# Kernel optimization log

Measured on AMD Instinct MI355X. Metric: run time of the kernel, lower is better.

## Reference

```python
import jax, jax.numpy as jnp
import numpy as np

B, D, NINC = 2097152, 16, 1000


def _make_map(key):
    # Build a valid adaptive map: per-dim monotone grid on [0,1] with NINC increments.
    w = jax.random.uniform(key, (D, NINC), dtype=jnp.float32) + 0.1  # positive widths
    inc = w / jnp.sum(w, axis=1, keepdims=True)                      # rows sum to 1
    grid = jnp.concatenate([jnp.zeros((D, 1), jnp.float32), jnp.cumsum(inc, axis=1)], axis=1)
    inc = grid[:, 1:] - grid[:, :-1]  # exact consistency: inc[d,i] = grid[d,i+1]-grid[d,i]
    return grid, inc


def setup_inputs() -> dict:
    key = jax.random.key(0)
    k1, k2 = jax.random.split(key)
    y = jax.random.uniform(k1, (B, D), dtype=jnp.float32)
    grid, inc = _make_map(k2)
    return {"y": y, "grid": grid, "inc": inc, "ninc": NINC}


def reference(y, grid, inc, ninc):
    # y: [B, D] in [0,1); grid: [D, ninc+1]; inc: [D, ninc]
    y_ninc = y * ninc                      # [B, D]
    iy = jnp.floor(y_ninc).astype(jnp.int32)
    dy_ninc = y_ninc - iy                  # fractional part within bin
    mask = iy < ninc                       # in-range bins (iy == ninc only when y == 1.0)
    iy_c = jnp.clip(iy, 0, ninc - 1)       # safe gather index
    d_idx = jnp.arange(y.shape[1])[None, :]  # [1, D]
    g = grid[d_idx, iy_c]                  # [B, D] left knot
    ig = inc[d_idx, iy_c]                  # [B, D] bin width
    # piecewise-linear affine map, predicated instead of boolean-mask scatter
    x = jnp.where(mask, g + ig * dy_ninc, grid[:, ninc][None, :])
    fac = jnp.where(mask, ig, inc[:, ninc - 1][None, :]) * ninc
    jac = jnp.prod(fac, axis=1)            # [B]
    return x, jac
```

## Files before the change

kernel.cpp:

```cpp
#include <hip/hip_runtime.h>


#define DIMS 16
#define NINC 1000
#define GROW (NINC + 1)
#define GTOT (DIMS * GROW)
#define BLOCK 1024
#define ROWS_PER_BLOCK 4096
#define NBLOCKS 512

__global__ __launch_bounds__(BLOCK, 8) void vegas_map_kernel(
    const float* __restrict__ y,
    const float* __restrict__ grid,
    float* __restrict__ x_out,
    float* __restrict__ jac_out,
    int B)
{
    __shared__ float sgrid[GTOT];

    {
        const float4* g4 = reinterpret_cast<const float4*>(grid);
        float4* s4 = reinterpret_cast<float4*>(sgrid);
        #pragma unroll
        for (int i = threadIdx.x; i < GTOT / 4; i += BLOCK)
            s4[i] = g4[i];
    }
    __syncthreads();

    const int base = blockIdx.x * ROWS_PER_BLOCK;

    #pragma unroll
    for (int it = 0; it < ROWS_PER_BLOCK / BLOCK; ++it) {
        const int b = base + it * BLOCK + threadIdx.x;
        if (b >= B) break;

        const float4* y4 = reinterpret_cast<const float4*>(y + (size_t)b * DIMS);
        float xs[DIMS];
        float jac = 1.0f;

        #pragma unroll
        for (int q = 0; q < 4; ++q) {
            float4 yv = y4[q];
            float ys[4] = {yv.x, yv.y, yv.z, yv.w};
            #pragma unroll
            for (int j = 0; j < 4; ++j) {
                const int d = q * 4 + j;
                float yn = ys[j] * (float)NINC;
                float fi = floorf(yn);
                int   iy = (int)fi;
                float dy = yn - (float)iy;
                int   iyc = iy < 0 ? 0 : (iy > NINC - 1 ? NINC - 1 : iy);
                const int sb = d * GROW + iyc;

                float xv, fac;
                if (iy < NINC) {
                    float g0 = sgrid[sb];
                    float g1 = sgrid[sb + 1];
                    float ig = g1 - g0;
                    xv  = g0 + ig * dy;
                    fac = ig;
                } else {
                    float gl = sgrid[d * GROW + NINC];
                    xv  = gl;
                    fac = gl - sgrid[d * GROW + NINC - 1];
                }
                xs[d] = xv;
                jac *= fac * (float)NINC;
            }
        }

        float4* x4 = reinterpret_cast<float4*>(x_out + (size_t)b * DIMS);
        float4 w0 = {xs[0],  xs[1],  xs[2],  xs[3]};
        float4 w1 = {xs[4],  xs[5],  xs[6],  xs[7]};
        float4 w2 = {xs[8],  xs[9],  xs[10], xs[11]};
        float4 w3 = {xs[12], xs[13], xs[14], xs[15]};
        x4[0] = w0;
        x4[1] = w1;
        x4[2] = w2;
        x4[3] = w3;
        jac_out[b] = jac;
    }
}

extern "C" void kernel_launch(void* const* d_in, const int* in_sizes, int n_in,
                              void* d_out, int out_size, void* d_ws, size_t ws_size,
                              hipStream_t stream) {
    const float* y    = (const float*)d_in[0];
    const float* grid = (const float*)d_in[1];

    const int B = in_sizes[0] / DIMS;

    float* x_out   = (float*)d_out;
    float* jac_out = x_out + (size_t)B * DIMS;

    vegas_map_kernel<<<NBLOCKS, BLOCK, 0, stream>>>(y, grid, x_out, jac_out, B);
}
```

Before: 266.1 us.

## Split each row across a 4-lane quad with DPP product reduction

Each row's 16 dimensions are now spread over four adjacent threads, each handling one float4. Global loads and stores of y and x become fully coalesced across the wavefront, where before each thread read 64 contiguous bytes. The per-row Jacobian is combined across the quad with DPP lane shuffles, and the out-of-range branch becomes a select on predicated values. The bounds check on B is removed, so correctness depends on B being a multiple of the rows per block.

```diff
diff --git a/kernel.cpp b/kernel.cpp
--- a/kernel.cpp
+++ b/kernel.cpp
@@ -6,8 +6,18 @@
 #define GROW (NINC + 1)
 #define GTOT (DIMS * GROW)
 #define BLOCK 1024
+#define NBLOCKS 512
 #define ROWS_PER_BLOCK 4096
-#define NBLOCKS 512
+#define QUADS_PER_BLOCK (BLOCK / 4)
+#define ITERS (ROWS_PER_BLOCK / QUADS_PER_BLOCK)
+
+__device__ __forceinline__ float quad_prod(float v) {
+    int t = __builtin_amdgcn_update_dpp(0, __float_as_int(v), 0xB1, 0xF, 0xF, true);
+    v *= __int_as_float(t);
+    t = __builtin_amdgcn_update_dpp(0, __float_as_int(v), 0x4E, 0xF, 0xF, true);
+    v *= __int_as_float(t);
+    return v;
+}
 
 __global__ __launch_bounds__(BLOCK, 8) void vegas_map_kernel(
     const float* __restrict__ y,
@@ -16,69 +26,64 @@
     float* __restrict__ jac_out,
     int B)
 {
-    __shared__ float sgrid[GTOT];
+    __shared__ __align__(16) float sgrid[GTOT];
 
     {
         const float4* g4 = reinterpret_cast<const float4*>(grid);
         float4* s4 = reinterpret_cast<float4*>(sgrid);
-        #pragma unroll
         for (int i = threadIdx.x; i < GTOT / 4; i += BLOCK)
             s4[i] = g4[i];
     }
     __syncthreads();
 
-    const int base = blockIdx.x * ROWS_PER_BLOCK;
+    const int quad   = threadIdx.x >> 2;
+    const int lane_d = threadIdx.x & 3;
+    const int d0     = lane_d * 4;
+    const int base   = blockIdx.x * ROWS_PER_BLOCK;
 
     #pragma unroll
-    for (int it = 0; it < ROWS_PER_BLOCK / BLOCK; ++it) {
-        const int b = base + it * BLOCK + threadIdx.x;
-        if (b >= B) break;
+    for (int it = 0; it < ITERS; ++it) {
+        const int row = base + it * QUADS_PER_BLOCK + quad;
 
-        const float4* y4 = reinterpret_cast<const float4*>(y + (size_t)b * DIMS);
-        float xs[DIMS];
-        float jac = 1.0f;
+        float4 yv = *reinterpret_cast<const float4*>(y + (size_t)row * DIMS + d0);
+        float ys[4] = {yv.x, yv.y, yv.z, yv.w};
 
+        int   addr[4];
+        float dy[4];
+        bool  inr[4];
         #pragma unroll
-        for (int q = 0; q < 4; ++q) {
-            float4 yv = y4[q];
-            float ys[4] = {yv.x, yv.y, yv.z, yv.w};
-            #pragma unroll
-            for (int j = 0; j < 4; ++j) {
-                const int d = q * 4 + j;
-                float yn = ys[j] * (float)NINC;
-                float fi = floorf(yn);
-                int   iy = (int)fi;
-                float dy = yn - (float)iy;
-                int   iyc = iy < 0 ? 0 : (iy > NINC - 1 ? NINC - 1 : iy);
-                const int sb = d * GROW + iyc;
-
-                float xv, fac;
-                if (iy < NINC) {
-                    float g0 = sgrid[sb];
-                    float g1 = sgrid[sb + 1];
-                    float ig = g1 - g0;
-                    xv  = g0 + ig * dy;
-                    fac = ig;
-                } else {
-                    float gl = sgrid[d * GROW + NINC];
-                    xv  = gl;
-                    fac = gl - sgrid[d * GROW + NINC - 1];
-                }
-                xs[d] = xv;
-                jac *= fac * (float)NINC;
-            }
+        for (int j = 0; j < 4; ++j) {
+            float yn = ys[j] * (float)NINC;
+            float fi = floorf(yn);
+            int   iy = (int)fi;
+            dy[j]  = yn - (float)iy;
+            inr[j] = iy < NINC;
+            int iyc = iy < 0 ? 0 : (iy > NINC - 1 ? NINC - 1 : iy);
+            addr[j] = (d0 + j) * GROW + iyc;
         }
 
-        float4* x4 = reinterpret_cast<float4*>(x_out + (size_t)b * DIMS);
-        float4 w0 = {xs[0],  xs[1],  xs[2],  xs[3]};
-        float4 w1 = {xs[4],  xs[5],  xs[6],  xs[7]};
-        float4 w2 = {xs[8],  xs[9],  xs[10], xs[11]};
-        float4 w3 = {xs[12], xs[13], xs[14], xs[15]};
-        x4[0] = w0;
-        x4[1] = w1;
-        x4[2] = w2;
-        x4[3] = w3;
-        jac_out[b] = jac;
+        float g0[4], g1[4];
+        #pragma unroll
+        for (int j = 0; j < 4; ++j) {
+            g0[j] = sgrid[addr[j]];
+            g1[j] = sgrid[addr[j] + 1];
+        }
+
+        float xs[4];
+        float jac = 1.0f;
+        #pragma unroll
+        for (int j = 0; j < 4; ++j) {
+            float ig = g1[j] - g0[j];
+            xs[j] = inr[j] ? fmaf(ig, dy[j], g0[j]) : g1[j];
+            jac *= ig * (float)NINC;
+        }
+
+        float jacq = quad_prod(jac);
+
+        float4 xw = {xs[0], xs[1], xs[2], xs[3]};
+        *reinterpret_cast<float4*>(x_out + (size_t)row * DIMS + d0) = xw;
+        if (lane_d == 0)
+            jac_out[row] = jacq;
     }
 }
 
```

Measured after the change: 253.7 us. -4.6%, faster.
